# Kernel optimization log

Hardware: AMD Instinct MI355X
Metric: run time of the kernel (lower is better)

The kernel has to match this reference:

```python
import jax, jax.numpy as jnp
import numpy as np

HEADS = 16
LN_EPS = 1e-5

def _ln(v, w, b):
    # LayerNorm over last dim (head dim s)
    mu = jnp.mean(v, axis=-1, keepdims=True)
    var = jnp.mean(jnp.square(v - mu), axis=-1, keepdims=True)
    return (v - mu) * jax.lax.rsqrt(var + LN_EPS) * w + b

def setup_inputs() -> dict:
    key = jax.random.key(0)
    ks = jax.random.split(key, 5)
    b, t, e = 2, 2048, 1024
    x = jax.random.normal(ks[0], (b, t, e), dtype=jnp.float32)
    scale = 0.02
    Wk = jax.random.normal(ks[1], (e, e), dtype=jnp.float32) * scale
    Wq = jax.random.normal(ks[2], (e, e), dtype=jnp.float32) * scale
    Wv = jax.random.normal(ks[3], (e, e), dtype=jnp.float32) * scale
    Wu = jax.random.normal(ks[4], (e, e), dtype=jnp.float32) * scale
    s = e // HEADS
    return {
        "x": x, "Wk": Wk, "Wq": Wq, "Wv": Wv, "Wu": Wu,
        "kln_w": jnp.ones((s,), jnp.float32), "kln_b": jnp.zeros((s,), jnp.float32),
        "qln_w": jnp.ones((s,), jnp.float32), "qln_b": jnp.zeros((s,), jnp.float32),
    }

def reference(x, Wk, Wq, Wv, Wu, kln_w, kln_b, qln_w, qln_b):
    b, t, e = x.shape
    h = HEADS
    s = e // h
    # nn.Linear: y = x @ W^T
    k = (x @ Wk.T).reshape(b, t, h, s)
    q = (x @ Wq.T).reshape(b, t, h, s)
    v = (x @ Wv.T).reshape(b, t, h, s)
    k = _ln(k, kln_w, kln_b)
    q = _ln(q, qln_w, qln_b)
    scalefactor = 1.0 / np.sqrt(s).astype(np.float32)
    # [b, h, t_q, t_k]
    dot = jnp.einsum('bqhs,bkhs->bhqk', q, k) * scalefactor
    causal = jnp.triu(jnp.ones((t, t), dtype=bool), k=1)  # mask strictly-upper (diag kept)
    dot = jnp.where(causal, -jnp.inf, dot)
    attn = jax.nn.softmax(dot, axis=-1)
    out = jnp.einsum('bhqk,bkhs->bqhs', attn, v).reshape(b, t, e)
    return out @ Wu.T
```

## Files before the change

kernel.cpp:

```cpp
#include <hip/hip_runtime.h>
#include <math.h>

#define T_SEQ 2048
#define E_DIM 1024
#define NH    16
#define HS    64
#define NB    2
#define M_ROWS 4096

typedef __attribute__((ext_vector_type(8))) short bf16x8;
typedef __attribute__((ext_vector_type(4))) float f32x4;

#define AS1 __attribute__((address_space(1)))
#define AS3 __attribute__((address_space(3)))

#define LOG2E 1.4426950408889634f

__device__ __forceinline__ ushort f2bf(float f) {
    union { float f; unsigned u; } c; c.f = f;
    unsigned r = c.u + 0x7fffu + ((c.u >> 16) & 1u);
    return (ushort)(r >> 16);
}
__device__ __forceinline__ ushort f2bf_trunc(float f) {
    union { float f; unsigned u; } c; c.f = f;
    return (ushort)(c.u >> 16);
}

__device__ __forceinline__ void load_lds16(const ushort* g, ushort* l) {
    __builtin_amdgcn_global_load_lds((const AS1 unsigned int*)g,
                                     (AS3 unsigned int*)l, 16, 0, 0);
}

__global__ __launch_bounds__(256) void cvt_all(
    const float* __restrict__ x,  const float* __restrict__ Wk,
    const float* __restrict__ Wq, const float* __restrict__ Wv,
    const float* __restrict__ Wu,
    ushort* __restrict__ xb,  ushort* __restrict__ Wkb,
    ushort* __restrict__ Wqb, ushort* __restrict__ Wvb,
    ushort* __restrict__ Wub)
{
    int i4 = blockIdx.x * 256 + threadIdx.x;
    int region = i4 >> 18;
    const float* src; ushort* dst; int off;
    if      (region < 4)  { src = x;  dst = xb;  off = i4; }
    else if (region == 4) { src = Wk; dst = Wkb; off = i4 - (4 << 18); }
    else if (region == 5) { src = Wq; dst = Wqb; off = i4 - (5 << 18); }
    else if (region == 6) { src = Wv; dst = Wvb; off = i4 - (6 << 18); }
    else                  { src = Wu; dst = Wub; off = i4 - (7 << 18); }
    float4 v = *(const float4*)(src + (size_t)off * 4);
    ushort4 o; o.x = f2bf(v.x); o.y = f2bf(v.y); o.z = f2bf(v.z); o.w = f2bf(v.w);
    *(ushort4*)(dst + (size_t)off * 4) = o;
}

__device__ __forceinline__ void gemm_core(
    const ushort* __restrict__ A, const ushort* __restrict__ W,
    ushort* As, ushort* Bs, f32x4 acc[4][4])
{
    const int tid  = threadIdx.x;
    const int lane = tid & 63, w = tid >> 6;
    const int quad = lane >> 4, l16 = lane & 15;
    const int wm = w & 1, wn = w >> 1;
    const int m0 = blockIdx.y * 128, n0 = blockIdx.x * 128;

    const int rl   = lane >> 2;
    const int gsw  = (lane & 3) ^ ((lane >> 3) & 3);
    const int fsw  = (l16 >> 1) & 3;

    const f32x4 zero = {0.f, 0.f, 0.f, 0.f};
#pragma unroll
    for (int mt = 0; mt < 4; ++mt)
#pragma unroll
        for (int nt = 0; nt < 4; ++nt) acc[mt][nt] = zero;

    for (int k0 = 0; k0 < E_DIM; k0 += 32) {
#pragma unroll
        for (int i = 0; i < 2; ++i) {
            int c = i * 4 + w;
            int row = c * 16 + rl;
            load_lds16(A + (size_t)(m0 + row) * E_DIM + k0 + gsw * 8, As + c * 512);
            load_lds16(W + (size_t)(n0 + row) * E_DIM + k0 + gsw * 8, Bs + c * 512);
        }
        __syncthreads();
        bf16x8 af[4], bfr[4];
#pragma unroll
        for (int mt = 0; mt < 4; ++mt)
            af[mt] = *(const bf16x8*)(As + (wm * 64 + mt * 16 + l16) * 32
                                      + ((quad ^ fsw) * 8));
#pragma unroll
        for (int nt = 0; nt < 4; ++nt)
            bfr[nt] = *(const bf16x8*)(Bs + (wn * 64 + nt * 16 + l16) * 32
                                       + ((quad ^ fsw) * 8));
#pragma unroll
        for (int mt = 0; mt < 4; ++mt)
#pragma unroll
            for (int nt = 0; nt < 4; ++nt)
                acc[mt][nt] = __builtin_amdgcn_mfma_f32_16x16x32_bf16(
                    af[mt], bfr[nt], acc[mt][nt], 0, 0, 0);
        __syncthreads();
    }
}

__global__ __launch_bounds__(256) void gemm_qkv(
    const ushort* __restrict__ A,
    const ushort* __restrict__ W0, const ushort* __restrict__ W1,
    const ushort* __restrict__ W2,
    ushort* __restrict__ Kb, ushort* __restrict__ Qb, ushort* __restrict__ Vt,
    const float* __restrict__ kw, const float* __restrict__ kbias,
    const float* __restrict__ qw, const float* __restrict__ qbias)
{
    __shared__ ushort As[128 * 32];
    __shared__ ushort Bs[128 * 32];
    const int z = blockIdx.z;
    const ushort* W = (z == 0) ? W0 : (z == 1) ? W1 : W2;
    f32x4 acc[4][4];
    gemm_core(A, W, As, Bs, acc);

    const int lane = threadIdx.x & 63, w = threadIdx.x >> 6;
    const int quad = lane >> 4, l16 = lane & 15;
    const int wm = w & 1, wn = w >> 1;
    const int m0 = blockIdx.y * 128, n0 = blockIdx.x * 128;
    const int row0 = m0 + wm * 64;
    const int col0 = n0 + wn * 64;

    if (z < 2) {
        ushort* C = z ? Qb : Kb;
        const float* lw = z ? qw : kw;
        const float* lb = z ? qbias : kbias;
        const float scale = z ? (0.125f * LOG2E) : 1.0f;
        float wv[4], bv_[4];
#pragma unroll
        for (int nt = 0; nt < 4; ++nt) {
            wv[nt]  = lw[nt * 16 + l16];
            bv_[nt] = lb[nt * 16 + l16];
        }
#pragma unroll
        for (int mt = 0; mt < 4; ++mt)
#pragma unroll
            for (int r = 0; r < 4; ++r) {
                float v[4], d[4];
#pragma unroll
                for (int nt = 0; nt < 4; ++nt) v[nt] = acc[mt][nt][r];
                float s = v[0] + v[1] + v[2] + v[3];
                s += __shfl_xor(s, 1); s += __shfl_xor(s, 2);
                s += __shfl_xor(s, 4); s += __shfl_xor(s, 8);
                float mu = s * (1.0f / 64.0f);
                float q2 = 0.f;
#pragma unroll
                for (int nt = 0; nt < 4; ++nt) { d[nt] = v[nt] - mu; q2 += d[nt] * d[nt]; }
                q2 += __shfl_xor(q2, 1); q2 += __shfl_xor(q2, 2);
                q2 += __shfl_xor(q2, 4); q2 += __shfl_xor(q2, 8);
                float rin = rsqrtf(q2 * (1.0f / 64.0f) + 1e-5f);
                int row = row0 + mt * 16 + quad * 4 + r;
#pragma unroll
                for (int nt = 0; nt < 4; ++nt)
                    C[(size_t)row * E_DIM + col0 + nt * 16 + l16] =
                        f2bf((d[nt] * rin * wv[nt] + bv_[nt]) * scale);
            }
    } else {
        const int bidx = m0 >> 11;
        const int hh   = col0 >> 6;
        const int t0   = (m0 & 2047) + wm * 64;
#pragma unroll
        for (int mt = 0; mt < 4; ++mt)
#pragma unroll
            for (int nt = 0; nt < 4; ++nt) {
                ushort4 pk = make_ushort4(f2bf(acc[mt][nt][0]), f2bf(acc[mt][nt][1]),
                                          f2bf(acc[mt][nt][2]), f2bf(acc[mt][nt][3]));
                size_t off = ((size_t)(bidx * NH + hh) * 64 + nt * 16 + l16) * T_SEQ
                             + t0 + mt * 16 + quad * 4;
                *(ushort4*)(Vt + off) = pk;
            }
    }
}

__global__ __launch_bounds__(256) void gemm_o(
    const ushort* __restrict__ A, const ushort* __restrict__ W,
    float* __restrict__ C)
{
    __shared__ ushort As[128 * 32];
    __shared__ ushort Bs[64 * 32];
    const int tid  = threadIdx.x;
    const int lane = tid & 63, w = tid >> 6;
    const int quad = lane >> 4, l16 = lane & 15;
    const int wm = w & 1, wn = w >> 1;
    const int m0 = blockIdx.y * 128, n0 = blockIdx.x * 64;

    const int rl  = lane >> 2;
    const int gsw = (lane & 3) ^ ((lane >> 3) & 3);
    const int fsw = (l16 >> 1) & 3;

    const f32x4 zero = {0.f, 0.f, 0.f, 0.f};
    f32x4 acc[4][2];
#pragma unroll
    for (int mt = 0; mt < 4; ++mt)
#pragma unroll
        for (int nt = 0; nt < 2; ++nt) acc[mt][nt] = zero;

    for (int k0 = 0; k0 < E_DIM; k0 += 32) {
#pragma unroll
        for (int i = 0; i < 2; ++i) {
            int c = i * 4 + w;
            int row = c * 16 + rl;
            load_lds16(A + (size_t)(m0 + row) * E_DIM + k0 + gsw * 8, As + c * 512);
        }
        {
            int row = w * 16 + rl;
            load_lds16(W + (size_t)(n0 + row) * E_DIM + k0 + gsw * 8, Bs + w * 512);
        }
        __syncthreads();
        bf16x8 af[4], bfr[2];
#pragma unroll
        for (int mt = 0; mt < 4; ++mt)
            af[mt] = *(const bf16x8*)(As + (wm * 64 + mt * 16 + l16) * 32
                                      + ((quad ^ fsw) * 8));
#pragma unroll
        for (int nt = 0; nt < 2; ++nt)
            bfr[nt] = *(const bf16x8*)(Bs + (wn * 32 + nt * 16 + l16) * 32
                                       + ((quad ^ fsw) * 8));
#pragma unroll
        for (int mt = 0; mt < 4; ++mt)
#pragma unroll
            for (int nt = 0; nt < 2; ++nt)
                acc[mt][nt] = __builtin_amdgcn_mfma_f32_16x16x32_bf16(
                    af[mt], bfr[nt], acc[mt][nt], 0, 0, 0);
        __syncthreads();
    }

    const int row0 = m0 + wm * 64;
    const int col0 = n0 + wn * 32;
#pragma unroll
    for (int mt = 0; mt < 4; ++mt)
#pragma unroll
        for (int nt = 0; nt < 2; ++nt)
#pragma unroll
            for (int r = 0; r < 4; ++r)
                C[(size_t)(row0 + mt * 16 + quad * 4 + r) * E_DIM
                  + col0 + nt * 16 + l16] = acc[mt][nt][r];
}

__global__ __launch_bounds__(256) void flash_attn3(
    const ushort* __restrict__ Qg, const ushort* __restrict__ Kg,
    const ushort* __restrict__ Vt, ushort* __restrict__ O)
{
    __shared__ ushort Ks[2][64 * 64];
    __shared__ ushort Vs[2][64 * 64];
    __shared__ ushort Ps[4][16 * 64];

    const int tid  = threadIdx.x;
    const int lane = tid & 63, w = tid >> 6;
    const int quad = lane >> 4, l16 = lane & 15;

    const int L = blockIdx.x;
    const int c = L & 255, s = L >> 8;
    const int q0 = c >> 5;
    const int bh = c & 31;
    const int qt = (s == 0) ? q0 : (s == 1) ? (15 - q0)
                 : (s == 2) ? (16 + q0) : (31 - q0);
    const int b = bh >> 4, h = bh & 15;

    const ushort* Qbase = Qg + ((size_t)b * T_SEQ) * E_DIM + h * HS;
    const ushort* Kbase = Kg + ((size_t)b * T_SEQ) * E_DIM + h * HS;
    const ushort* Vbase = Vt + ((size_t)bh * HS) * T_SEQ;

    const int rloc = lane >> 3;
    const int gswc = (lane & 7) ^ rloc;
    const int sw   = l16 & 7;

    bf16x8 aq[2];
#pragma unroll
    for (int ks = 0; ks < 2; ++ks)
        aq[ks] = *(const bf16x8*)(Qbase + (size_t)(qt * 64 + w * 16 + l16) * E_DIM
                                  + ks * 32 + quad * 8);

    const f32x4 zero = {0.f, 0.f, 0.f, 0.f};
    f32x4 o_acc[4];
#pragma unroll
    for (int dt = 0; dt < 4; ++dt) o_acc[dt] = zero;
    float l_acc[4] = {0.f, 0.f, 0.f, 0.f};

#pragma unroll
    for (int i = 0; i < 2; ++i) {
        int cc = w * 2 + i, row = cc * 8 + rloc;
        load_lds16(Kbase + (size_t)row * E_DIM + gswc * 8, Ks[0] + cc * 512);
        load_lds16(Vbase + (size_t)row * T_SEQ + gswc * 8, Vs[0] + cc * 512);
    }

    const float M8 = 8.0f * LOG2E;

    for (int jt = 0; jt <= qt; ++jt) {
        const int buf = jt & 1;
        __syncthreads();
        if (jt < qt) {
#pragma unroll
            for (int i = 0; i < 2; ++i) {
                int cc = w * 2 + i, row = cc * 8 + rloc;
                load_lds16(Kbase + (size_t)(jt + 1) * 64 * E_DIM
                           + (size_t)row * E_DIM + gswc * 8, Ks[buf ^ 1] + cc * 512);
                load_lds16(Vbase + (size_t)row * T_SEQ + (jt + 1) * 64 + gswc * 8,
                           Vs[buf ^ 1] + cc * 512);
            }
        }

        f32x4 sa[4];
#pragma unroll
        for (int nt = 0; nt < 4; ++nt) sa[nt] = zero;
#pragma unroll
        for (int ks = 0; ks < 2; ++ks) {
            int cp = ((ks * 4 + quad) ^ sw) * 8;
#pragma unroll
            for (int nt = 0; nt < 4; ++nt) {
                bf16x8 bk = *(const bf16x8*)(Ks[buf] + (nt * 16 + l16) * 64 + cp);
                sa[nt] = __builtin_amdgcn_mfma_f32_16x16x32_bf16(aq[ks], bk, sa[nt], 0, 0, 0);
            }
        }

        if (jt == qt) {
#pragma unroll
            for (int nt = 0; nt < 4; ++nt)
#pragma unroll
                for (int r = 0; r < 4; ++r)
                    if (nt * 16 + l16 > w * 16 + quad * 4 + r) sa[nt][r] = -1e30f;
        }

#pragma unroll
        for (int nt = 0; nt < 4; ++nt)
#pragma unroll
            for (int r = 0; r < 4; ++r) {
                float p = __builtin_amdgcn_exp2f(sa[nt][r] - M8);
                sa[nt][r] = p;
                l_acc[r] += p;
            }

#pragma unroll
        for (int nt = 0; nt < 4; ++nt)
#pragma unroll
            for (int r = 0; r < 4; ++r) {
                int row = quad * 4 + r;
                int cp  = (nt * 2 + (l16 >> 3)) ^ (row & 7);
                Ps[w][row * 64 + cp * 8 + (l16 & 7)] = f2bf_trunc(sa[nt][r]);
            }

#pragma unroll
        for (int ks = 0; ks < 2; ++ks) {
            int cp = ((ks * 4 + quad) ^ sw) * 8;
            bf16x8 ap = *(const bf16x8*)(Ps[w] + l16 * 64 + cp);
#pragma unroll
            for (int dt = 0; dt < 4; ++dt) {
                bf16x8 bv = *(const bf16x8*)(Vs[buf] + (dt * 16 + l16) * 64 + cp);
                o_acc[dt] = __builtin_amdgcn_mfma_f32_16x16x32_bf16(ap, bv, o_acc[dt], 0, 0, 0);
            }
        }
    }

#pragma unroll
    for (int r = 0; r < 4; ++r) {
        float Lr = l_acc[r];
        Lr += __shfl_xor(Lr, 1); Lr += __shfl_xor(Lr, 2);
        Lr += __shfl_xor(Lr, 4); Lr += __shfl_xor(Lr, 8);
        float inv = 1.0f / Lr;
        int trow = qt * 64 + w * 16 + quad * 4 + r;
#pragma unroll
        for (int dt = 0; dt < 4; ++dt)
            O[((size_t)b * T_SEQ + trow) * E_DIM + h * HS + dt * 16 + l16] =
                f2bf(o_acc[dt][r] * inv);
    }
}

extern "C" void kernel_launch(void* const* d_in, const int* in_sizes, int n_in,
                              void* d_out, int out_size, void* d_ws, size_t ws_size,
                              hipStream_t stream) {
    const float* x     = (const float*)d_in[0];
    const float* Wk    = (const float*)d_in[1];
    const float* Wq    = (const float*)d_in[2];
    const float* Wv    = (const float*)d_in[3];
    const float* Wu    = (const float*)d_in[4];
    const float* kln_w = (const float*)d_in[5];
    const float* kln_b = (const float*)d_in[6];
    const float* qln_w = (const float*)d_in[7];
    const float* qln_b = (const float*)d_in[8];
    float* out = (float*)d_out;

    const size_t NE = (size_t)M_ROWS * E_DIM;
    const size_t NW = (size_t)E_DIM * E_DIM;
    ushort* xb  = (ushort*)d_ws;
    ushort* Wkb = xb  + NE;
    ushort* Wqb = Wkb + NW;
    ushort* Wvb = Wqb + NW;
    ushort* Wub = Wvb + NW;
    ushort* Kb  = Wub + NW;
    ushort* Qb  = Kb  + NE;
    ushort* Vt  = Qb  + NE;
    ushort* Ob  = Vt  + NE;

    cvt_all<<<8192, 256, 0, stream>>>(x, Wk, Wq, Wv, Wu, xb, Wkb, Wqb, Wvb, Wub);

    gemm_qkv<<<dim3(E_DIM / 128, M_ROWS / 128, 3), 256, 0, stream>>>(
        xb, Wkb, Wqb, Wvb, Kb, Qb, Vt, kln_w, kln_b, qln_w, qln_b);

    flash_attn3<<<1024, 256, 0, stream>>>(Qb, Kb, Vt, Ob);

    gemm_o<<<dim3(E_DIM / 64, M_ROWS / 128), 256, 0, stream>>>(Ob, Wub, out);
}
```

Measured before the change: 189.3 us.

## Double query rows per attention wave and retile QKV GEMM to 128x64 blocks

The flash attention kernel now gives each wave 32 query rows (128 per block) instead of 16, so each K/V fragment loaded from LDS feeds twice as many MFMAs. The grid shrinks from 1024 to 512 blocks, with waves skipping KV tiles entirely above their causal diagonal. The QKV GEMM switches from 128x128 tiles with a z-dimension to 128x64 tiles over a flattened 3072-column grid, sharing one core routine with the output projection GEMM. The trade-offs are more registers per wave in attention, fewer blocks to spread across CUs, and more work imbalance between waves inside a block.

```diff
diff --git a/kernel.cpp b/kernel.cpp
--- a/kernel.cpp
+++ b/kernel.cpp
@@ -52,15 +52,13 @@
     *(ushort4*)(dst + (size_t)off * 4) = o;
 }
 
-__device__ __forceinline__ void gemm_core(
+__device__ __forceinline__ void gemm_core64(
     const ushort* __restrict__ A, const ushort* __restrict__ W,
-    ushort* As, ushort* Bs, f32x4 acc[4][4])
+    int m0, int n0, ushort* As, ushort* Bs, f32x4 acc[2][4])
 {
     const int tid  = threadIdx.x;
     const int lane = tid & 63, w = tid >> 6;
     const int quad = lane >> 4, l16 = lane & 15;
-    const int wm = w & 1, wn = w >> 1;
-    const int m0 = blockIdx.y * 128, n0 = blockIdx.x * 128;
 
     const int rl   = lane >> 2;
     const int gsw  = (lane & 3) ^ ((lane >> 3) & 3);
@@ -68,30 +66,33 @@
 
     const f32x4 zero = {0.f, 0.f, 0.f, 0.f};
 #pragma unroll
-    for (int mt = 0; mt < 4; ++mt)
+    for (int mt = 0; mt < 2; ++mt)
 #pragma unroll
         for (int nt = 0; nt < 4; ++nt) acc[mt][nt] = zero;
 
     for (int k0 = 0; k0 < E_DIM; k0 += 32) {
 #pragma unroll
         for (int i = 0; i < 2; ++i) {
-            int c = i * 4 + w;
+            int c = w + i * 4;
             int row = c * 16 + rl;
             load_lds16(A + (size_t)(m0 + row) * E_DIM + k0 + gsw * 8, As + c * 512);
-            load_lds16(W + (size_t)(n0 + row) * E_DIM + k0 + gsw * 8, Bs + c * 512);
+        }
+        {
+            int row = w * 16 + rl;
+            load_lds16(W + (size_t)(n0 + row) * E_DIM + k0 + gsw * 8, Bs + w * 512);
         }
         __syncthreads();
-        bf16x8 af[4], bfr[4];
-#pragma unroll
-        for (int mt = 0; mt < 4; ++mt)
-            af[mt] = *(const bf16x8*)(As + (wm * 64 + mt * 16 + l16) * 32
+        bf16x8 af[2], bfr[4];
+#pragma unroll
+        for (int mt = 0; mt < 2; ++mt)
+            af[mt] = *(const bf16x8*)(As + (w * 32 + mt * 16 + l16) * 32
                                       + ((quad ^ fsw) * 8));
 #pragma unroll
         for (int nt = 0; nt < 4; ++nt)
-            bfr[nt] = *(const bf16x8*)(Bs + (wn * 64 + nt * 16 + l16) * 32
+            bfr[nt] = *(const bf16x8*)(Bs + (nt * 16 + l16) * 32
                                        + ((quad ^ fsw) * 8));
 #pragma unroll
-        for (int mt = 0; mt < 4; ++mt)
+        for (int mt = 0; mt < 2; ++mt)
 #pragma unroll
             for (int nt = 0; nt < 4; ++nt)
                 acc[mt][nt] = __builtin_amdgcn_mfma_f32_16x16x32_bf16(
@@ -109,18 +110,19 @@
     const float* __restrict__ qw, const float* __restrict__ qbias)
 {
     __shared__ ushort As[128 * 32];
-    __shared__ ushort Bs[128 * 32];
-    const int z = blockIdx.z;
+    __shared__ ushort Bs[64 * 32];
+    const int n0g = blockIdx.x * 64;
+    const int z   = n0g >> 10;
+    const int n0  = n0g & 1023;
+    const int m0  = blockIdx.y * 128;
     const ushort* W = (z == 0) ? W0 : (z == 1) ? W1 : W2;
-    f32x4 acc[4][4];
-    gemm_core(A, W, As, Bs, acc);
+
+    f32x4 acc[2][4];
+    gemm_core64(A, W, m0, n0, As, Bs, acc);
 
     const int lane = threadIdx.x & 63, w = threadIdx.x >> 6;
     const int quad = lane >> 4, l16 = lane & 15;
-    const int wm = w & 1, wn = w >> 1;
-    const int m0 = blockIdx.y * 128, n0 = blockIdx.x * 128;
-    const int row0 = m0 + wm * 64;
-    const int col0 = n0 + wn * 64;
+    const int row0 = m0 + w * 32;
 
     if (z < 2) {
         ushort* C = z ? Qb : Kb;
@@ -134,7 +136,7 @@
             bv_[nt] = lb[nt * 16 + l16];
         }
 #pragma unroll
-        for (int mt = 0; mt < 4; ++mt)
+        for (int mt = 0; mt < 2; ++mt)
 #pragma unroll
             for (int r = 0; r < 4; ++r) {
                 float v[4], d[4];
@@ -153,15 +155,15 @@
                 int row = row0 + mt * 16 + quad * 4 + r;
 #pragma unroll
                 for (int nt = 0; nt < 4; ++nt)
-                    C[(size_t)row * E_DIM + col0 + nt * 16 + l16] =
+                    C[(size_t)row * E_DIM + n0 + nt * 16 + l16] =
                         f2bf((d[nt] * rin * wv[nt] + bv_[nt]) * scale);
             }
     } else {
         const int bidx = m0 >> 11;
-        const int hh   = col0 >> 6;
-        const int t0   = (m0 & 2047) + wm * 64;
-#pragma unroll
-        for (int mt = 0; mt < 4; ++mt)
+        const int hh   = n0 >> 6;
+        const int t0   = (m0 & 2047) + w * 32;
+#pragma unroll
+        for (int mt = 0; mt < 2; ++mt)
 #pragma unroll
             for (int nt = 0; nt < 4; ++nt) {
                 ushort4 pk = make_ushort4(f2bf(acc[mt][nt][0]), f2bf(acc[mt][nt][1]),
@@ -179,72 +181,30 @@
 {
     __shared__ ushort As[128 * 32];
     __shared__ ushort Bs[64 * 32];
-    const int tid  = threadIdx.x;
-    const int lane = tid & 63, w = tid >> 6;
+    const int m0 = blockIdx.y * 128, n0 = blockIdx.x * 64;
+    f32x4 acc[2][4];
+    gemm_core64(A, W, m0, n0, As, Bs, acc);
+
+    const int lane = threadIdx.x & 63, w = threadIdx.x >> 6;
     const int quad = lane >> 4, l16 = lane & 15;
-    const int wm = w & 1, wn = w >> 1;
-    const int m0 = blockIdx.y * 128, n0 = blockIdx.x * 64;
-
-    const int rl  = lane >> 2;
-    const int gsw = (lane & 3) ^ ((lane >> 3) & 3);
-    const int fsw = (l16 >> 1) & 3;
-
-    const f32x4 zero = {0.f, 0.f, 0.f, 0.f};
-    f32x4 acc[4][2];
-#pragma unroll
-    for (int mt = 0; mt < 4; ++mt)
-#pragma unroll
-        for (int nt = 0; nt < 2; ++nt) acc[mt][nt] = zero;
-
-    for (int k0 = 0; k0 < E_DIM; k0 += 32) {
-#pragma unroll
-        for (int i = 0; i < 2; ++i) {
-            int c = i * 4 + w;
-            int row = c * 16 + rl;
-            load_lds16(A + (size_t)(m0 + row) * E_DIM + k0 + gsw * 8, As + c * 512);
-        }
-        {
-            int row = w * 16 + rl;
-            load_lds16(W + (size_t)(n0 + row) * E_DIM + k0 + gsw * 8, Bs + w * 512);
-        }
-        __syncthreads();
-        bf16x8 af[4], bfr[2];
-#pragma unroll
-        for (int mt = 0; mt < 4; ++mt)
-            af[mt] = *(const bf16x8*)(As + (wm * 64 + mt * 16 + l16) * 32
-                                      + ((quad ^ fsw) * 8));
-#pragma unroll
-        for (int nt = 0; nt < 2; ++nt)
-            bfr[nt] = *(const bf16x8*)(Bs + (wn * 32 + nt * 16 + l16) * 32
-                                       + ((quad ^ fsw) * 8));
-#pragma unroll
-        for (int mt = 0; mt < 4; ++mt)
-#pragma unroll
-            for (int nt = 0; nt < 2; ++nt)
-                acc[mt][nt] = __builtin_amdgcn_mfma_f32_16x16x32_bf16(
-                    af[mt], bfr[nt], acc[mt][nt], 0, 0, 0);
-        __syncthreads();
-    }
-
-    const int row0 = m0 + wm * 64;
-    const int col0 = n0 + wn * 32;
-#pragma unroll
-    for (int mt = 0; mt < 4; ++mt)
-#pragma unroll
-        for (int nt = 0; nt < 2; ++nt)
+    const int row0 = m0 + w * 32;
+#pragma unroll
+    for (int mt = 0; mt < 2; ++mt)
+#pragma unroll
+        for (int nt = 0; nt < 4; ++nt)
 #pragma unroll
             for (int r = 0; r < 4; ++r)
                 C[(size_t)(row0 + mt * 16 + quad * 4 + r) * E_DIM
-                  + col0 + nt * 16 + l16] = acc[mt][nt][r];
-}
-
-__global__ __launch_bounds__(256) void flash_attn3(
+                  + n0 + nt * 16 + l16] = acc[mt][nt][r];
+}
+
+__global__ __launch_bounds__(256) void flash_attn4(
     const ushort* __restrict__ Qg, const ushort* __restrict__ Kg,
     const ushort* __restrict__ Vt, ushort* __restrict__ O)
 {
     __shared__ ushort Ks[2][64 * 64];
     __shared__ ushort Vs[2][64 * 64];
-    __shared__ ushort Ps[4][16 * 64];
+    __shared__ ushort Ps[4][32 * 64];
 
     const int tid  = threadIdx.x;
     const int lane = tid & 63, w = tid >> 6;
@@ -254,8 +214,7 @@
     const int c = L & 255, s = L >> 8;
     const int q0 = c >> 5;
     const int bh = c & 31;
-    const int qt = (s == 0) ? q0 : (s == 1) ? (15 - q0)
-                 : (s == 2) ? (16 + q0) : (31 - q0);
+    const int qt = s ? (15 - q0) : q0;
     const int b = bh >> 4, h = bh & 15;
 
     const ushort* Qbase = Qg + ((size_t)b * T_SEQ) * E_DIM + h * HS;
@@ -266,17 +225,23 @@
     const int gswc = (lane & 7) ^ rloc;
     const int sw   = l16 & 7;
 
-    bf16x8 aq[2];
-#pragma unroll
-    for (int ks = 0; ks < 2; ++ks)
-        aq[ks] = *(const bf16x8*)(Qbase + (size_t)(qt * 64 + w * 16 + l16) * E_DIM
-                                  + ks * 32 + quad * 8);
+    const int base_w = qt * 128 + w * 32;
+
+    bf16x8 aq[2][2];
+#pragma unroll
+    for (int u = 0; u < 2; ++u)
+#pragma unroll
+        for (int ks = 0; ks < 2; ++ks)
+            aq[u][ks] = *(const bf16x8*)(Qbase
+                + (size_t)(base_w + u * 16 + l16) * E_DIM + ks * 32 + quad * 8);
 
     const f32x4 zero = {0.f, 0.f, 0.f, 0.f};
-    f32x4 o_acc[4];
-#pragma unroll
-    for (int dt = 0; dt < 4; ++dt) o_acc[dt] = zero;
-    float l_acc[4] = {0.f, 0.f, 0.f, 0.f};
+    f32x4 o_acc[2][4];
+#pragma unroll
+    for (int u = 0; u < 2; ++u)
+#pragma unroll
+        for (int dt = 0; dt < 4; ++dt) o_acc[u][dt] = zero;
+    float l_acc[2][4] = {{0.f,0.f,0.f,0.f},{0.f,0.f,0.f,0.f}};
 
 #pragma unroll
     for (int i = 0; i < 2; ++i) {
@@ -286,11 +251,12 @@
     }
 
     const float M8 = 8.0f * LOG2E;
-
-    for (int jt = 0; jt <= qt; ++jt) {
+    const int ntiles = 2 * qt + 2;
+
+    for (int jt = 0; jt < ntiles; ++jt) {
         const int buf = jt & 1;
         __syncthreads();
-        if (jt < qt) {
+        if (jt + 1 < ntiles) {
 #pragma unroll
             for (int i = 0; i < 2; ++i) {
                 int cc = w * 2 + i, row = cc * 8 + rloc;
@@ -301,69 +267,93 @@
             }
         }
 
-        f32x4 sa[4];
-#pragma unroll
-        for (int nt = 0; nt < 4; ++nt) sa[nt] = zero;
+        if (jt * 64 > base_w + 31) continue;
+
+        f32x4 sa[2][4];
+#pragma unroll
+        for (int u = 0; u < 2; ++u)
+#pragma unroll
+            for (int nt = 0; nt < 4; ++nt) sa[u][nt] = zero;
 #pragma unroll
         for (int ks = 0; ks < 2; ++ks) {
             int cp = ((ks * 4 + quad) ^ sw) * 8;
-#pragma unroll
-            for (int nt = 0; nt < 4; ++nt) {
-                bf16x8 bk = *(const bf16x8*)(Ks[buf] + (nt * 16 + l16) * 64 + cp);
-                sa[nt] = __builtin_amdgcn_mfma_f32_16x16x32_bf16(aq[ks], bk, sa[nt], 0, 0, 0);
-            }
-        }
-
-        if (jt == qt) {
+            bf16x8 bk[4];
 #pragma unroll
             for (int nt = 0; nt < 4; ++nt)
-#pragma unroll
-                for (int r = 0; r < 4; ++r)
-                    if (nt * 16 + l16 > w * 16 + quad * 4 + r) sa[nt][r] = -1e30f;
-        }
-
-#pragma unroll
-        for (int nt = 0; nt < 4; ++nt)
-#pragma unroll
-            for (int r = 0; r < 4; ++r) {
-                float p = __builtin_amdgcn_exp2f(sa[nt][r] - M8);
-                sa[nt][r] = p;
-                l_acc[r] += p;
-            }
-
-#pragma unroll
-        for (int nt = 0; nt < 4; ++nt)
-#pragma unroll
-            for (int r = 0; r < 4; ++r) {
-                int row = quad * 4 + r;
-                int cp  = (nt * 2 + (l16 >> 3)) ^ (row & 7);
-                Ps[w][row * 64 + cp * 8 + (l16 & 7)] = f2bf_trunc(sa[nt][r]);
-            }
+                bk[nt] = *(const bf16x8*)(Ks[buf] + (nt * 16 + l16) * 64 + cp);
+#pragma unroll
+            for (int u = 0; u < 2; ++u)
+#pragma unroll
+                for (int nt = 0; nt < 4; ++nt)
+                    sa[u][nt] = __builtin_amdgcn_mfma_f32_16x16x32_bf16(
+                        aq[u][ks], bk[nt], sa[u][nt], 0, 0, 0);
+        }
+
+        if (jt * 64 + 63 > base_w) {
+#pragma unroll
+            for (int u = 0; u < 2; ++u)
+#pragma unroll
+                for (int nt = 0; nt < 4; ++nt)
+#pragma unroll
+                    for (int r = 0; r < 4; ++r)
+                        if (jt * 64 + nt * 16 + l16 >
+                            base_w + u * 16 + quad * 4 + r) sa[u][nt][r] = -1e30f;
+        }
+
+#pragma unroll
+        for (int u = 0; u < 2; ++u)
+#pragma unroll
+            for (int nt = 0; nt < 4; ++nt)
+#pragma unroll
+                for (int r = 0; r < 4; ++r) {
+                    float p = __builtin_amdgcn_exp2f(sa[u][nt][r] - M8);
+                    sa[u][nt][r] = p;
+                    l_acc[u][r] += p;
+                }
+
+#pragma unroll
+        for (int u = 0; u < 2; ++u)
+#pragma unroll
+            for (int nt = 0; nt < 4; ++nt)
+#pragma unroll
+                for (int r = 0; r < 4; ++r) {
+                    int row = u * 16 + quad * 4 + r;
+                    int cp2 = (nt * 2 + (l16 >> 3)) ^ (row & 7);
+                    Ps[w][row * 64 + cp2 * 8 + (l16 & 7)] = f2bf_trunc(sa[u][nt][r]);
+                }
 
 #pragma unroll
         for (int ks = 0; ks < 2; ++ks) {
             int cp = ((ks * 4 + quad) ^ sw) * 8;
-            bf16x8 ap = *(const bf16x8*)(Ps[w] + l16 * 64 + cp);
-#pragma unroll
-            for (int dt = 0; dt < 4; ++dt) {
-                bf16x8 bv = *(const bf16x8*)(Vs[buf] + (dt * 16 + l16) * 64 + cp);
-                o_acc[dt] = __builtin_amdgcn_mfma_f32_16x16x32_bf16(ap, bv, o_acc[dt], 0, 0, 0);
+            bf16x8 bv[4];
+#pragma unroll
+            for (int dt = 0; dt < 4; ++dt)
+                bv[dt] = *(const bf16x8*)(Vs[buf] + (dt * 16 + l16) * 64 + cp);
+#pragma unroll
+            for (int u = 0; u < 2; ++u) {
+                bf16x8 ap = *(const bf16x8*)(Ps[w] + (u * 16 + l16) * 64 + cp);
+#pragma unroll
+                for (int dt = 0; dt < 4; ++dt)
+                    o_acc[u][dt] = __builtin_amdgcn_mfma_f32_16x16x32_bf16(
+                        ap, bv[dt], o_acc[u][dt], 0, 0, 0);
             }
         }
     }
 
 #pragma unroll
-    for (int r = 0; r < 4; ++r) {
-        float Lr = l_acc[r];
-        Lr += __shfl_xor(Lr, 1); Lr += __shfl_xor(Lr, 2);
-        Lr += __shfl_xor(Lr, 4); Lr += __shfl_xor(Lr, 8);
-        float inv = 1.0f / Lr;
-        int trow = qt * 64 + w * 16 + quad * 4 + r;
-#pragma unroll
-        for (int dt = 0; dt < 4; ++dt)
-            O[((size_t)b * T_SEQ + trow) * E_DIM + h * HS + dt * 16 + l16] =
-                f2bf(o_acc[dt][r] * inv);
-    }
+    for (int u = 0; u < 2; ++u)
+#pragma unroll
+        for (int r = 0; r < 4; ++r) {
+            float Lr = l_acc[u][r];
+            Lr += __shfl_xor(Lr, 1); Lr += __shfl_xor(Lr, 2);
+            Lr += __shfl_xor(Lr, 4); Lr += __shfl_xor(Lr, 8);
+            float inv = 1.0f / Lr;
+            int trow = base_w + u * 16 + quad * 4 + r;
+#pragma unroll
+            for (int dt = 0; dt < 4; ++dt)
+                O[((size_t)b * T_SEQ + trow) * E_DIM + h * HS + dt * 16 + l16] =
+                    f2bf(o_acc[u][dt][r] * inv);
+        }
 }
 
 extern "C" void kernel_launch(void* const* d_in, const int* in_sizes, int n_in,
@@ -394,10 +384,10 @@
 
     cvt_all<<<8192, 256, 0, stream>>>(x, Wk, Wq, Wv, Wu, xb, Wkb, Wqb, Wvb, Wub);
 
-    gemm_qkv<<<dim3(E_DIM / 128, M_ROWS / 128, 3), 256, 0, stream>>>(
+    gemm_qkv<<<dim3(3 * E_DIM / 64, M_ROWS / 128), 256, 0, stream>>>(
         xb, Wkb, Wqb, Wvb, Kb, Qb, Vt, kln_w, kln_b, qln_w, qln_b);
 
-    flash_attn3<<<1024, 256, 0, stream>>>(Qb, Kb, Vt, Ob);
+    flash_attn4<<<512, 256, 0, stream>>>(Qb, Kb, Vt, Ob);
 
     gemm_o<<<dim3(E_DIM / 64, M_ROWS / 128), 256, 0, stream>>>(Ob, Wub, out);
 }
```

Result: slower. 204.9 us (+8.2%).

## Compute transposed S in attention so P stays in registers, dropping LDS round-trip

Applied to the files above, without the earlier changes.

The attention kernel swaps the MFMA operands to produce S transposed, so each lane holds probabilities for one query row across key positions. Those values are packed directly into bf16x4 operands for a 16x16x16 MFMA against V, which removes the per-warp LDS buffer for P and its write/read round-trip. The row-sum reduction and output store are restructured to match, with vectorized ushort4 stores, and launch bounds now request 4 blocks per CU. The trade-off is twice as many smaller MFMA instructions for PV and narrower V reads from LDS, which may cost more LDS traffic or bank conflicts. The GEMM core gets a small refactor to pass the tile origin explicitly.

```diff
diff --git a/kernel.cpp b/kernel.cpp
--- a/kernel.cpp
+++ b/kernel.cpp
@@ -9,12 +9,17 @@
 #define M_ROWS 4096
 
 typedef __attribute__((ext_vector_type(8))) short bf16x8;
+typedef __attribute__((ext_vector_type(4))) short bf16x4;
 typedef __attribute__((ext_vector_type(4))) float f32x4;
 
 #define AS1 __attribute__((address_space(1)))
 #define AS3 __attribute__((address_space(3)))
 
 #define LOG2E 1.4426950408889634f
+
+__device__ __forceinline__ f32x4 mfma16(bf16x4 a, bf16x4 b, f32x4 c) {
+    return __builtin_amdgcn_mfma_f32_16x16x16bf16_1k(a, b, c, 0, 0, 0);
+}
 
 __device__ __forceinline__ ushort f2bf(float f) {
     union { float f; unsigned u; } c; c.f = f;
@@ -54,13 +59,12 @@
 
 __device__ __forceinline__ void gemm_core(
     const ushort* __restrict__ A, const ushort* __restrict__ W,
-    ushort* As, ushort* Bs, f32x4 acc[4][4])
+    int m0, int n0, ushort* As, ushort* Bs, f32x4 acc[4][4])
 {
     const int tid  = threadIdx.x;
     const int lane = tid & 63, w = tid >> 6;
     const int quad = lane >> 4, l16 = lane & 15;
     const int wm = w & 1, wn = w >> 1;
-    const int m0 = blockIdx.y * 128, n0 = blockIdx.x * 128;
 
     const int rl   = lane >> 2;
     const int gsw  = (lane & 3) ^ ((lane >> 3) & 3);
@@ -112,13 +116,13 @@
     __shared__ ushort Bs[128 * 32];
     const int z = blockIdx.z;
     const ushort* W = (z == 0) ? W0 : (z == 1) ? W1 : W2;
+    const int m0 = blockIdx.y * 128, n0 = blockIdx.x * 128;
     f32x4 acc[4][4];
-    gemm_core(A, W, As, Bs, acc);
+    gemm_core(A, W, m0, n0, As, Bs, acc);
 
     const int lane = threadIdx.x & 63, w = threadIdx.x >> 6;
     const int quad = lane >> 4, l16 = lane & 15;
     const int wm = w & 1, wn = w >> 1;
-    const int m0 = blockIdx.y * 128, n0 = blockIdx.x * 128;
     const int row0 = m0 + wm * 64;
     const int col0 = n0 + wn * 64;
 
@@ -238,13 +242,12 @@
                   + col0 + nt * 16 + l16] = acc[mt][nt][r];
 }
 
-__global__ __launch_bounds__(256) void flash_attn3(
+__global__ __launch_bounds__(256, 4) void flash_attn5(
     const ushort* __restrict__ Qg, const ushort* __restrict__ Kg,
     const ushort* __restrict__ Vt, ushort* __restrict__ O)
 {
     __shared__ ushort Ks[2][64 * 64];
     __shared__ ushort Vs[2][64 * 64];
-    __shared__ ushort Ps[4][16 * 64];
 
     const int tid  = threadIdx.x;
     const int lane = tid & 63, w = tid >> 6;
@@ -276,7 +279,7 @@
     f32x4 o_acc[4];
 #pragma unroll
     for (int dt = 0; dt < 4; ++dt) o_acc[dt] = zero;
-    float l_acc[4] = {0.f, 0.f, 0.f, 0.f};
+    float l_acc = 0.f;
 
 #pragma unroll
     for (int i = 0; i < 2; ++i) {
@@ -310,7 +313,7 @@
 #pragma unroll
             for (int nt = 0; nt < 4; ++nt) {
                 bf16x8 bk = *(const bf16x8*)(Ks[buf] + (nt * 16 + l16) * 64 + cp);
-                sa[nt] = __builtin_amdgcn_mfma_f32_16x16x32_bf16(aq[ks], bk, sa[nt], 0, 0, 0);
+                sa[nt] = __builtin_amdgcn_mfma_f32_16x16x32_bf16(bk, aq[ks], sa[nt], 0, 0, 0);
             }
         }
 
@@ -319,50 +322,43 @@
             for (int nt = 0; nt < 4; ++nt)
 #pragma unroll
                 for (int r = 0; r < 4; ++r)
-                    if (nt * 16 + l16 > w * 16 + quad * 4 + r) sa[nt][r] = -1e30f;
-        }
-
+                    if (nt * 16 + quad * 4 + r > w * 16 + l16) sa[nt][r] = -1e30f;
+        }
+
+        bf16x4 bp[4];
 #pragma unroll
         for (int nt = 0; nt < 4; ++nt)
 #pragma unroll
             for (int r = 0; r < 4; ++r) {
                 float p = __builtin_amdgcn_exp2f(sa[nt][r] - M8);
-                sa[nt][r] = p;
-                l_acc[r] += p;
-            }
-
-#pragma unroll
-        for (int nt = 0; nt < 4; ++nt)
-#pragma unroll
-            for (int r = 0; r < 4; ++r) {
-                int row = quad * 4 + r;
-                int cp  = (nt * 2 + (l16 >> 3)) ^ (row & 7);
-                Ps[w][row * 64 + cp * 8 + (l16 & 7)] = f2bf_trunc(sa[nt][r]);
-            }
-
-#pragma unroll
-        for (int ks = 0; ks < 2; ++ks) {
-            int cp = ((ks * 4 + quad) ^ sw) * 8;
-            bf16x8 ap = *(const bf16x8*)(Ps[w] + l16 * 64 + cp);
+                l_acc += p;
+                bp[nt][r] = (short)f2bf_trunc(p);
+            }
+
+#pragma unroll
+        for (int kt = 0; kt < 4; ++kt) {
+            const int tt = kt * 16 + quad * 4;
+            const int ch = tt >> 3, el = tt & 7;
 #pragma unroll
             for (int dt = 0; dt < 4; ++dt) {
-                bf16x8 bv = *(const bf16x8*)(Vs[buf] + (dt * 16 + l16) * 64 + cp);
-                o_acc[dt] = __builtin_amdgcn_mfma_f32_16x16x32_bf16(ap, bv, o_acc[dt], 0, 0, 0);
-            }
-        }
-    }
-
-#pragma unroll
-    for (int r = 0; r < 4; ++r) {
-        float Lr = l_acc[r];
-        Lr += __shfl_xor(Lr, 1); Lr += __shfl_xor(Lr, 2);
-        Lr += __shfl_xor(Lr, 4); Lr += __shfl_xor(Lr, 8);
-        float inv = 1.0f / Lr;
-        int trow = qt * 64 + w * 16 + quad * 4 + r;
-#pragma unroll
-        for (int dt = 0; dt < 4; ++dt)
-            O[((size_t)b * T_SEQ + trow) * E_DIM + h * HS + dt * 16 + l16] =
-                f2bf(o_acc[dt][r] * inv);
+                const int vd = dt * 16 + l16;
+                bf16x4 va = *(const bf16x4*)(Vs[buf] + vd * 64
+                                             + ((ch ^ (vd & 7)) << 3) + el);
+                o_acc[dt] = mfma16(va, bp[kt], o_acc[dt]);
+            }
+        }
+    }
+
+    l_acc += __shfl_xor(l_acc, 16);
+    l_acc += __shfl_xor(l_acc, 32);
+    const float inv = 1.0f / l_acc;
+    const int trow = qt * 64 + w * 16 + l16;
+#pragma unroll
+    for (int dt = 0; dt < 4; ++dt) {
+        ushort4 pk = make_ushort4(f2bf(o_acc[dt][0] * inv), f2bf(o_acc[dt][1] * inv),
+                                  f2bf(o_acc[dt][2] * inv), f2bf(o_acc[dt][3] * inv));
+        *(ushort4*)(O + ((size_t)b * T_SEQ + trow) * E_DIM + h * HS
+                    + dt * 16 + quad * 4) = pk;
     }
 }
 
@@ -397,7 +393,7 @@
     gemm_qkv<<<dim3(E_DIM / 128, M_ROWS / 128, 3), 256, 0, stream>>>(
         xb, Wkb, Wqb, Wvb, Kb, Qb, Vt, kln_w, kln_b, qln_w, qln_b);
 
-    flash_attn3<<<1024, 256, 0, stream>>>(Qb, Kb, Vt, Ob);
+    flash_attn5<<<1024, 256, 0, stream>>>(Qb, Kb, Vt, Ob);
 
     gemm_o<<<dim3(E_DIM / 64, M_ROWS / 128), 256, 0, stream>>>(Ob, Wub, out);
 }
```

After: 181.9 us. 1.04x faster.
